# Kernel optimization log

Hardware: AMD Instinct MI355X
Metric: run time of the kernel (lower is better)

The kernel has to match this reference:

```python
import jax, jax.numpy as jnp
import numpy as np

NUM_HEADS = 16
HEAD_DIM = 64
D_MODEL = NUM_HEADS * HEAD_DIM
DFF = 4096
LN_EPS = 1e-3  # keras LayerNormalization default epsilon


def layer_norm(x, gamma, beta):
    mu = jnp.mean(x, axis=-1, keepdims=True)
    var = jnp.mean(jnp.square(x - mu), axis=-1, keepdims=True)
    return (x - mu) * jax.lax.rsqrt(var + LN_EPS) * gamma + beta


def setup_inputs() -> dict:
    key = jax.random.key(0)
    ks = jax.random.split(key, 8)
    N, T = 2, 2048
    s = 0.02
    return {
        "x": jax.random.normal(ks[0], (N, T, D_MODEL), dtype=jnp.float32),
        "mask": jnp.ones((N, T), dtype=jnp.float32),
        "w_qkv": jax.random.normal(ks[1], (D_MODEL, 3 * D_MODEL), dtype=jnp.float32) * s,
        "b_qkv": jnp.zeros((3 * D_MODEL,), dtype=jnp.float32),
        "w_ff": jax.random.normal(ks[2], (D_MODEL, DFF), dtype=jnp.float32) * s,
        "b_ff": jnp.zeros((DFF,), dtype=jnp.float32),
        "w_out": jax.random.normal(ks[3], (DFF, D_MODEL), dtype=jnp.float32) * s,
        "b_out": jnp.zeros((D_MODEL,), dtype=jnp.float32),
        "ln1_g": jnp.ones((D_MODEL,), dtype=jnp.float32),
        "ln1_b": jnp.zeros((D_MODEL,), dtype=jnp.float32),
        "ln2_g": jnp.ones((D_MODEL,), dtype=jnp.float32),
        "ln2_b": jnp.zeros((D_MODEL,), dtype=jnp.float32),
    }


def reference(x, mask, w_qkv, b_qkv, w_ff, b_ff, w_out, b_out, ln1_g, ln1_b, ln2_g, ln2_b):
    N, T, _ = x.shape
    H, D = NUM_HEADS, HEAD_DIM
    # --- MHA ---
    qkv = x @ w_qkv + b_qkv                     # [N, T, 3*H*D]
    qkv = qkv.reshape(N, T, H, D, 3)
    qkv = jnp.transpose(qkv, (4, 0, 2, 1, 3))   # [3, N, H, T, D]
    q, k, v = qkv[0], qkv[1], qkv[2]
    logits = jnp.einsum('nhqd,nhkd->nhqk', q, k) * (1.0 / (D ** 0.5))
    # NB: faithful to original: mask[:, None, :, None] masks the QUERY axis
    logits = logits + (1.0 - mask[:, None, :, None]) * -1e9
    attn = jax.nn.softmax(logits, axis=-1)
    ctx = jnp.einsum('nhqk,nhkd->nhqd', attn, v)  # [N, H, T, D]
    ctx = jnp.transpose(ctx, (0, 2, 1, 3)).reshape(N, T, H * D)
    # dropout_rc1: identity (training=False)
    h = layer_norm(x + ctx, ln1_g, ln1_b)
    # --- FFN ---
    ff = jax.nn.relu(h @ w_ff + b_ff)             # [N, T, DFF]
    out = layer_norm(h + ff @ w_out + b_out, ln2_g, ln2_b)
    return out
```

## Files before the change

### kernel.cpp

```cpp
#include <hip/hip_runtime.h>
#include <hip/hip_fp8.h>
#include <stdint.h>

#define DM    1024
#define DFFN  4096
#define NTOK  4096
#define TT    2048
#define NHEAD 16
#define HD    64
#define LN_EPS 1e-3f
#define QSCALE 0.18033688011112042f

typedef float  f32x4  __attribute__((ext_vector_type(4)));
typedef __bf16 bf16x8 __attribute__((ext_vector_type(8)));

using void_as1 = __attribute__((address_space(1))) void;
using void_as3 = __attribute__((address_space(3))) void;

__device__ __forceinline__ void g2l16(const void* g, void* l) {
    __builtin_amdgcn_global_load_lds((const void_as1*)g, (void_as3*)l, 16, 0, 0);
}

__device__ __forceinline__ unsigned short f2bf(float f) {
    unsigned u = __builtin_bit_cast(unsigned, f);
    u += 0x7FFFu + ((u >> 16) & 1u);
    return (unsigned short)(u >> 16);
}

__device__ __forceinline__ float fexp2(float x) {
#if __has_builtin(__builtin_amdgcn_exp2f)
    return __builtin_amdgcn_exp2f(x);
#else
    return exp2f(x);
#endif
}

template <bool HI>
__device__ __forceinline__ unsigned cvt2fp8(float a, float b, unsigned old) {
#if __has_builtin(__builtin_amdgcn_cvt_pk_fp8_f32)
    return (unsigned)__builtin_amdgcn_cvt_pk_fp8_f32(a, b, (int)old, HI);
#else
    __hip_fp8_e4m3 ta(a), tb(b);
    unsigned w = (unsigned)ta.__x | ((unsigned)tb.__x << 8);
    return HI ? ((old & 0x0000FFFFu) | (w << 16)) : ((old & 0xFFFF0000u) | w);
#endif
}

__device__ __forceinline__ unsigned char f2fp8(float f) {
    return (unsigned char)(cvt2fp8<false>(f, 0.f, 0u) & 0xffu);
}

__global__ __launch_bounds__(256) void cast_bf16_kernel(
    const float* __restrict__ in, unsigned short* __restrict__ out, int n4) {
    int i = blockIdx.x * 256 + threadIdx.x;
    if (i < n4) {
        float4 v = ((const float4*)in)[i];
        ushort4 o;
        o.x = f2bf(v.x); o.y = f2bf(v.y); o.z = f2bf(v.z); o.w = f2bf(v.w);
        ((ushort4*)out)[i] = o;
    }
}

__global__ __launch_bounds__(256) void transpose_cast_kernel(
    const float* __restrict__ w, unsigned short* __restrict__ wT, int K, int Nc) {
    __shared__ float tile[32][33];
    int tx = threadIdx.x & 31, ty = threadIdx.x >> 5;
    int n0 = blockIdx.x * 32, k0 = blockIdx.y * 32;
#pragma unroll
    for (int i = 0; i < 4; ++i)
        tile[ty + 8 * i][tx] = w[(size_t)(k0 + ty + 8 * i) * Nc + (n0 + tx)];
    __syncthreads();
#pragma unroll
    for (int i = 0; i < 4; ++i)
        wT[(size_t)(n0 + ty + 8 * i) * K + (k0 + tx)] = f2bf(tile[tx][ty + 8 * i]);
}

template <int EPI>
__global__ __launch_bounds__(256, 4) void gemm_bt_kernel(
    const unsigned short* __restrict__ A,
    const unsigned short* __restrict__ Bt,
    const float* __restrict__ bias,
    unsigned short* __restrict__ oq,
    unsigned short* __restrict__ ok,
    unsigned short* __restrict__ ov,
    float* __restrict__ of,
    int K, int Ksplit) {
    __shared__ unsigned short As[128 * 64];
    __shared__ unsigned short Bs[128 * 64];
    const int tid  = threadIdx.x;
    const int wave = tid >> 6, lane = tid & 63;
    const int quad = lane >> 4, l16 = lane & 15;
    const int sw = l16 & 7;
    const int wm = wave >> 1, wn = wave & 1;
    const int nBase = blockIdx.x * 128, mBase = blockIdx.y * 128;
    const int kb = blockIdx.z * Ksplit, ke = kb + Ksplit;

    f32x4 acc[4][4] = {};

    for (int k0 = kb; k0 < ke; k0 += 64) {
#pragma unroll
        for (int i = 0; i < 4; ++i) {
            const int chunk = i * 256 + tid;
            const int row = chunk >> 3, kc = chunk & 7;
            const int kl = kc ^ (row & 7);
            g2l16(A  + (size_t)(mBase + row) * K + (k0 + kl * 8),
                  (char*)As + (size_t)(i * 256 + wave * 64) * 16);
        }
#pragma unroll
        for (int i = 0; i < 4; ++i) {
            const int chunk = i * 256 + tid;
            const int row = chunk >> 3, kc = chunk & 7;
            const int kl = kc ^ (row & 7);
            g2l16(Bt + (size_t)(nBase + row) * K + (k0 + kl * 8),
                  (char*)Bs + (size_t)(i * 256 + wave * 64) * 16);
        }
        __syncthreads();
#pragma unroll
        for (int ks = 0; ks < 2; ++ks) {
            bf16x8 af[4], bfr[4];
#pragma unroll
            for (int i = 0; i < 4; ++i)
                af[i] = *(const bf16x8*)(const void*)(
                    As + (wm * 64 + i * 16 + l16) * 64 + (((ks * 4 + quad) ^ sw) << 3));
#pragma unroll
            for (int j = 0; j < 4; ++j)
                bfr[j] = *(const bf16x8*)(const void*)(
                    Bs + (wn * 64 + j * 16 + l16) * 64 + (((ks * 4 + quad) ^ sw) << 3));
#pragma unroll
            for (int i = 0; i < 4; ++i)
#pragma unroll
                for (int j = 0; j < 4; ++j)
                    acc[i][j] = __builtin_amdgcn_mfma_f32_16x16x32_bf16(af[i], bfr[j], acc[i][j], 0, 0, 0);
        }
        __syncthreads();
    }

    float* dst2 = (EPI == 2) ? (blockIdx.z ? (float*)ov : of) : nullptr;

#pragma unroll
    for (int i = 0; i < 4; ++i) {
        const int rbase = mBase + wm * 64 + i * 16 + quad * 4;
#pragma unroll
        for (int j = 0; j < 4; ++j) {
            const int col = nBase + wn * 64 + j * 16 + l16;
            const float bv = (EPI == 2) ? 0.0f : bias[col];
#pragma unroll
            for (int r = 0; r < 4; ++r) {
                const int row = rbase + r;
                const float v = acc[i][j][r] + bv;
                if (EPI == 0) {
                    const int h = col / 192;
                    const int rem = col - h * 192;
                    const int d = rem / 3;
                    const int s = rem - d * 3;
                    const int n = row >> 11, t = row & (TT - 1);
                    const int nh = n * NHEAD + h;
                    if (s == 0)
                        ((unsigned char*)oq)[((size_t)nh * TT + t) * HD + d] = f2fp8(v);
                    else if (s == 1)
                        ((unsigned char*)ok)[((size_t)nh * TT + t) * HD + d] = f2fp8(v);
                    else {
                        const int tl = t & 127;
                        const int tp = ((tl & 15) << 3) | (tl >> 4);
                        ((unsigned char*)ov)[((size_t)nh * HD + d) * TT + (t & ~127) + tp] = f2fp8(v);
                    }
                } else if (EPI == 1) {
                    oq[(size_t)row * DFFN + col] = f2bf(fmaxf(v, 0.0f));
                } else {
                    dst2[(size_t)row * DM + col] = v;
                }
            }
        }
    }
}

#define PST 136
__global__ __launch_bounds__(512, 4) void attn_kernel(
    const unsigned char* __restrict__ q,
    const unsigned char* __restrict__ k,
    const unsigned char* __restrict__ vt,
    float* __restrict__ ctx) {
    __shared__ __align__(16) unsigned char Ks[128 * 64];
    __shared__ __align__(16) unsigned char Vs[64 * 128];
    __shared__ __align__(16) unsigned char Plds[8][16 * PST];
    const int tid  = threadIdx.x;
    const int wave = tid >> 6, lane = tid & 63;
    const int quad = lane >> 4, l16 = lane & 15;
    const int nh = blockIdx.x & 31;
    const int qt = blockIdx.x >> 5;
    const unsigned char* qh = q  + (size_t)nh * TT * HD;
    const unsigned char* kh = k  + (size_t)nh * TT * HD;
    const unsigned char* vh = vt + (size_t)nh * HD * TT;

    const int qrow = qt * 128 + wave * 16;
    const long qa0 = *(const long*)(const void*)(qh + (size_t)(qrow + l16) * HD + quad * 8);
    const long qa1 = *(const long*)(const void*)(qh + (size_t)(qrow + l16) * HD + 32 + quad * 8);

    f32x4 o[4] = {};
    f32x4 rs = {};
    unsigned char* pw = &Plds[wave][0];
    const int sw2 = (l16 >> 1) & 3;

    for (int kt = 0; kt < TT; kt += 128) {
        {
            const int r = wave * 16 + (lane >> 2);
            const int lc = (lane & 3) ^ ((lane >> 3) & 3);
            g2l16(kh + (size_t)(kt + r) * HD + lc * 16, (char*)Ks + wave * 1024);
        }
        {
            const int d = wave * 8 + (lane >> 3);
            const int lc = (lane & 7) ^ (d & 7);
            g2l16(vh + (size_t)d * TT + kt + lc * 16, (char*)Vs + wave * 1024);
        }
        __syncthreads();

        f32x4 s[8];
#pragma unroll
        for (int c = 0; c < 8; ++c) {
            const int r = c * 16 + l16;
            const long kb0 = *(const long*)(const void*)(
                Ks + r * 64 + ((((quad >> 1) ^ sw2)) << 4) + ((quad & 1) << 3));
            const long kb1 = *(const long*)(const void*)(
                Ks + r * 64 + (((2 + (quad >> 1)) ^ sw2) << 4) + ((quad & 1) << 3));
            f32x4 z = {};
            z = __builtin_amdgcn_mfma_f32_16x16x32_fp8_fp8(qa0, kb0, z, 0, 0, 0);
            s[c] = __builtin_amdgcn_mfma_f32_16x16x32_fp8_fp8(qa1, kb1, z, 0, 0, 0);
        }
#pragma unroll
        for (int c = 0; c < 8; ++c)
#pragma unroll
            for (int r = 0; r < 4; ++r) {
                float p = fexp2(s[c][r] * QSCALE);
                s[c][r] = p;
                rs[r] += p;
            }
#pragma unroll
        for (int r = 0; r < 4; ++r) {
            const int row = quad * 4 + r;
            unsigned lo = cvt2fp8<false>(s[0][r], s[1][r], 0u);
            lo = cvt2fp8<true>(s[2][r], s[3][r], lo);
            unsigned hi = cvt2fp8<false>(s[4][r], s[5][r], 0u);
            hi = cvt2fp8<true>(s[6][r], s[7][r], hi);
            uint2 wv; wv.x = lo; wv.y = hi;
            *(uint2*)(void*)(pw + row * PST + l16 * 8) = wv;
        }
        asm volatile("s_waitcnt lgkmcnt(0)" ::: "memory");
#pragma unroll
        for (int kc = 0; kc < 4; ++kc) {
            const long pa = *(const long*)(const void*)(pw + l16 * PST + kc * 32 + quad * 8);
#pragma unroll
            for (int dc = 0; dc < 4; ++dc) {
                const int physc = (kc * 2 + (quad >> 1)) ^ (l16 & 7);
                const long vb = *(const long*)(const void*)(
                    Vs + (dc * 16 + l16) * 128 + physc * 16 + ((quad & 1) << 3));
                o[dc] = __builtin_amdgcn_mfma_f32_16x16x32_fp8_fp8(pa, vb, o[dc], 0, 0, 0);
            }
        }
        __syncthreads();
    }

    const int n = nh >> 4, h = nh & 15;
#pragma unroll
    for (int r = 0; r < 4; ++r) {
        float t = rs[r];
        t += __shfl_xor(t, 1, 64);
        t += __shfl_xor(t, 2, 64);
        t += __shfl_xor(t, 4, 64);
        t += __shfl_xor(t, 8, 64);
        const float inv = 1.0f / t;
        const int trow = qrow + quad * 4 + r;
        float* op = ctx + ((size_t)(n * TT + trow)) * DM + h * HD;
#pragma unroll
        for (int dc = 0; dc < 4; ++dc)
            op[dc * 16 + l16] = o[dc][r] * inv;
    }
}

__global__ __launch_bounds__(256) void add_ln_kernel(
    const float* __restrict__ a, const float* __restrict__ b,
    const float* __restrict__ c, const float* __restrict__ cbias,
    const float* __restrict__ gamma, const float* __restrict__ beta,
    float* __restrict__ outf, unsigned short* __restrict__ outb) {
    const int row = blockIdx.x;
    const int tid = threadIdx.x;
    const int lane = tid & 63, wave = tid >> 6;
    const float4 av = ((const float4*)(a + (size_t)row * DM))[tid];
    const float4 bv = ((const float4*)(b + (size_t)row * DM))[tid];
    float4 x;
    x.x = av.x + bv.x; x.y = av.y + bv.y; x.z = av.z + bv.z; x.w = av.w + bv.w;
    if (c) {
        const float4 cv = ((const float4*)(c + (size_t)row * DM))[tid];
        const float4 cb = ((const float4*)cbias)[tid];
        x.x += cv.x + cb.x; x.y += cv.y + cb.y; x.z += cv.z + cb.z; x.w += cv.w + cb.w;
    }
    float s = x.x + x.y + x.z + x.w;
    float q = x.x * x.x + x.y * x.y + x.z * x.z + x.w * x.w;
#pragma unroll
    for (int off = 1; off < 64; off <<= 1) {
        s += __shfl_xor(s, off, 64);
        q += __shfl_xor(q, off, 64);
    }
    __shared__ float sh[8];
    if (lane == 0) { sh[wave] = s; sh[4 + wave] = q; }
    __syncthreads();
    s = sh[0] + sh[1] + sh[2] + sh[3];
    q = sh[4] + sh[5] + sh[6] + sh[7];
    const float mu = s * (1.0f / DM);
    const float var = q * (1.0f / DM) - mu * mu;
    const float rstd = rsqrtf(var + LN_EPS);
    const float4 g4 = ((const float4*)gamma)[tid];
    const float4 b4 = ((const float4*)beta)[tid];
    float4 o;
    o.x = (x.x - mu) * rstd * g4.x + b4.x;
    o.y = (x.y - mu) * rstd * g4.y + b4.y;
    o.z = (x.z - mu) * rstd * g4.z + b4.z;
    o.w = (x.w - mu) * rstd * g4.w + b4.w;
    ((float4*)(outf + (size_t)row * DM))[tid] = o;
    if (outb) {
        ushort4 ob;
        ob.x = f2bf(o.x); ob.y = f2bf(o.y); ob.z = f2bf(o.z); ob.w = f2bf(o.w);
        ((ushort4*)(outb + (size_t)row * DM))[tid] = ob;
    }
}

extern "C" void kernel_launch(void* const* d_in, const int* in_sizes, int n_in,
                              void* d_out, int out_size, void* d_ws, size_t ws_size,
                              hipStream_t stream) {
    const float* x     = (const float*)d_in[0];
    const float* w_qkv = (const float*)d_in[2];
    const float* b_qkv = (const float*)d_in[3];
    const float* w_ff  = (const float*)d_in[4];
    const float* b_ff  = (const float*)d_in[5];
    const float* w_out = (const float*)d_in[6];
    const float* b_out = (const float*)d_in[7];
    const float* ln1_g = (const float*)d_in[8];
    const float* ln1_b = (const float*)d_in[9];
    const float* ln2_g = (const float*)d_in[10];
    const float* ln2_b = (const float*)d_in[11];

    char* ws = (char*)d_ws;
    unsigned short* xb    = (unsigned short*)(ws);
    unsigned short* wqkvT = (unsigned short*)(ws + 8388608);
    unsigned short* wffT  = (unsigned short*)(ws + 14680064);
    unsigned short* woutT = (unsigned short*)(ws + 23068672);
    unsigned char*  qb    = (unsigned char*)(ws + 31457280);
    unsigned char*  kb    = (unsigned char*)(ws + 39845888);
    unsigned char*  vtb   = (unsigned char*)(ws + 48234496);
    float*          ctx   = (float*)(ws + 56623104);
    float*          hbuf  = (float*)(ws + 73400320);
    unsigned short* hb    = (unsigned short*)(ws + 90177536);
    unsigned short* ffb   = (unsigned short*)(ws + 98566144);
    float*          tmp   = (float*)(ws + 132120576);

    cast_bf16_kernel<<<(NTOK * DM / 4 + 255) / 256, 256, 0, stream>>>(x, xb, NTOK * DM / 4);
    transpose_cast_kernel<<<dim3(3072 / 32, DM / 32), 256, 0, stream>>>(w_qkv, wqkvT, DM, 3072);
    transpose_cast_kernel<<<dim3(DFFN / 32, DM / 32), 256, 0, stream>>>(w_ff, wffT, DM, DFFN);
    transpose_cast_kernel<<<dim3(DM / 32, DFFN / 32), 256, 0, stream>>>(w_out, woutT, DFFN, DM);

    gemm_bt_kernel<0><<<dim3(3072 / 128, NTOK / 128), 256, 0, stream>>>(
        xb, wqkvT, b_qkv, (unsigned short*)qb, (unsigned short*)kb,
        (unsigned short*)vtb, nullptr, DM, DM);

    attn_kernel<<<512, 512, 0, stream>>>(qb, kb, vtb, ctx);

    add_ln_kernel<<<NTOK, 256, 0, stream>>>(x, ctx, nullptr, nullptr,
                                            ln1_g, ln1_b, hbuf, hb);

    gemm_bt_kernel<1><<<dim3(DFFN / 128, NTOK / 128), 256, 0, stream>>>(
        hb, wffT, b_ff, ffb, nullptr, nullptr, nullptr, DM, DM);

    gemm_bt_kernel<2><<<dim3(DM / 128, NTOK / 128, 2), 256, 0, stream>>>(
        ffb, woutT, nullptr, nullptr, nullptr, (unsigned short*)ctx, tmp, DFFN, DFFN / 2);

    add_ln_kernel<<<NTOK, 256, 0, stream>>>(hbuf, tmp, ctx, b_out,
                                            ln2_g, ln2_b, (float*)d_out, nullptr);
}
```

Before: 328.4 us.

## Run QKV projection in FP8 and give each attention wave 32 query rows

The QKV projection now runs as a dedicated FP8 GEMM. Its input is cast to FP8, and the weights are pre-permuted so each output column maps directly to q/k/v, head and dim, which makes the scatter epilogue cheaper. The attention kernel now uses 256 threads per block, and each wave processes two 16-row query sub-tiles against the shared K/V tiles. This doubles K/V reuse per LDS load, and the P buffer uses a swizzled layout instead of padding. The risks are lower QKV accuracy from FP8 inputs and weights, and higher register pressure in attention.

```diff
diff --git a/kernel.cpp b/kernel.cpp
--- a/kernel.cpp
+++ b/kernel.cpp
@@ -13,6 +13,7 @@
 
 typedef float  f32x4  __attribute__((ext_vector_type(4)));
 typedef __bf16 bf16x8 __attribute__((ext_vector_type(8)));
+typedef long   lx2    __attribute__((ext_vector_type(2)));
 
 using void_as1 = __attribute__((address_space(1))) void;
 using void_as3 = __attribute__((address_space(3))) void;
@@ -50,14 +51,14 @@
     return (unsigned char)(cvt2fp8<false>(f, 0.f, 0u) & 0xffu);
 }
 
-__global__ __launch_bounds__(256) void cast_bf16_kernel(
-    const float* __restrict__ in, unsigned short* __restrict__ out, int n4) {
+__global__ __launch_bounds__(256) void cast_fp8_kernel(
+    const float* __restrict__ in, unsigned char* __restrict__ out, int n4) {
     int i = blockIdx.x * 256 + threadIdx.x;
     if (i < n4) {
         float4 v = ((const float4*)in)[i];
-        ushort4 o;
-        o.x = f2bf(v.x); o.y = f2bf(v.y); o.z = f2bf(v.z); o.w = f2bf(v.w);
-        ((ushort4*)out)[i] = o;
+        unsigned p = cvt2fp8<false>(v.x, v.y, 0u);
+        p = cvt2fp8<true>(v.z, v.w, p);
+        ((unsigned*)out)[i] = p;
     }
 }
 
@@ -75,15 +76,120 @@
         wT[(size_t)(n0 + ty + 8 * i) * K + (k0 + tx)] = f2bf(tile[tx][ty + 8 * i]);
 }
 
+__global__ __launch_bounds__(256) void transpose_qkv_fp8_kernel(
+    const float* __restrict__ w, unsigned char* __restrict__ wT) {
+    __shared__ float tile[32][33];
+    int tx = threadIdx.x & 31, ty = threadIdx.x >> 5;
+    int c0 = blockIdx.x * 32, k0 = blockIdx.y * 32;
+#pragma unroll
+    for (int i = 0; i < 4; ++i)
+        tile[ty + 8 * i][tx] = w[(size_t)(k0 + ty + 8 * i) * 3072 + (c0 + tx)];
+    __syncthreads();
+#pragma unroll
+    for (int i = 0; i < 4; ++i) {
+        const int col = c0 + ty + 8 * i;
+        const int h = col / 192;
+        const int rem = col - h * 192;
+        const int d = rem / 3;
+        const int s = rem - d * 3;
+        const int colp = s * 1024 + h * 64 + d;
+        wT[(size_t)colp * 1024 + (k0 + tx)] = f2fp8(tile[tx][ty + 8 * i]);
+    }
+}
+
+__global__ __launch_bounds__(256, 4) void gemm_qkv_fp8_kernel(
+    const unsigned char* __restrict__ A,
+    const unsigned char* __restrict__ Bt,
+    const float* __restrict__ bias,
+    unsigned char* __restrict__ oq,
+    unsigned char* __restrict__ ok,
+    unsigned char* __restrict__ ov) {
+    __shared__ __align__(16) unsigned char As[128 * 64];
+    __shared__ __align__(16) unsigned char Bs[128 * 64];
+    const int tid  = threadIdx.x;
+    const int wave = tid >> 6, lane = tid & 63;
+    const int quad = lane >> 4, l16 = lane & 15;
+    const int sw2 = (l16 >> 1) & 3;
+    const int wm = wave >> 1, wn = wave & 1;
+    const int nBase = blockIdx.x * 128, mBase = blockIdx.y * 128;
+
+    f32x4 acc[4][4] = {};
+
+    for (int k0 = 0; k0 < 1024; k0 += 64) {
+#pragma unroll
+        for (int i = 0; i < 2; ++i) {
+            const int chunk = i * 256 + tid;
+            const int row = chunk >> 2, p = chunk & 3;
+            const int l = p ^ ((row >> 1) & 3);
+            g2l16(A + (size_t)(mBase + row) * 1024 + (k0 + l * 16),
+                  (char*)As + (size_t)(i * 256 + wave * 64) * 16);
+        }
+#pragma unroll
+        for (int i = 0; i < 2; ++i) {
+            const int chunk = i * 256 + tid;
+            const int row = chunk >> 2, p = chunk & 3;
+            const int l = p ^ ((row >> 1) & 3);
+            g2l16(Bt + (size_t)(nBase + row) * 1024 + (k0 + l * 16),
+                  (char*)Bs + (size_t)(i * 256 + wave * 64) * 16);
+        }
+        __syncthreads();
+        lx2 af[4], bf[4];
+#pragma unroll
+        for (int i = 0; i < 4; ++i)
+            af[i] = *(const lx2*)(const void*)(
+                As + (wm * 64 + i * 16 + l16) * 64 + ((quad ^ sw2) << 4));
+#pragma unroll
+        for (int j = 0; j < 4; ++j)
+            bf[j] = *(const lx2*)(const void*)(
+                Bs + (wn * 64 + j * 16 + l16) * 64 + ((quad ^ sw2) << 4));
+#pragma unroll
+        for (int i = 0; i < 4; ++i)
+#pragma unroll
+            for (int j = 0; j < 4; ++j) {
+                acc[i][j] = __builtin_amdgcn_mfma_f32_16x16x32_fp8_fp8(af[i].x, bf[j].x, acc[i][j], 0, 0, 0);
+                acc[i][j] = __builtin_amdgcn_mfma_f32_16x16x32_fp8_fp8(af[i].y, bf[j].y, acc[i][j], 0, 0, 0);
+            }
+        __syncthreads();
+    }
+
+#pragma unroll
+    for (int i = 0; i < 4; ++i) {
+        const int rbase = mBase + wm * 64 + i * 16 + quad * 4;
+#pragma unroll
+        for (int j = 0; j < 4; ++j) {
+            const int colp = nBase + wn * 64 + j * 16 + l16;
+            const int s = colp >> 10;
+            const int h = (colp >> 6) & 15;
+            const int d = colp & 63;
+            const float bv = bias[h * 192 + d * 3 + s];
+#pragma unroll
+            for (int r = 0; r < 4; ++r) {
+                const int row = rbase + r;
+                const float v = acc[i][j][r] + bv;
+                const int n = row >> 11, t = row & (TT - 1);
+                const int nh = n * NHEAD + h;
+                if (s == 0)
+                    oq[((size_t)nh * TT + t) * HD + d] = f2fp8(v);
+                else if (s == 1)
+                    ok[((size_t)nh * TT + t) * HD + d] = f2fp8(v);
+                else {
+                    const int tl = t & 127;
+                    const int tp = ((tl & 15) << 3) | (tl >> 4);
+                    ov[((size_t)nh * HD + d) * TT + (t & ~127) + tp] = f2fp8(v);
+                }
+            }
+        }
+    }
+}
+
 template <int EPI>
 __global__ __launch_bounds__(256, 4) void gemm_bt_kernel(
     const unsigned short* __restrict__ A,
     const unsigned short* __restrict__ Bt,
     const float* __restrict__ bias,
-    unsigned short* __restrict__ oq,
-    unsigned short* __restrict__ ok,
-    unsigned short* __restrict__ ov,
+    unsigned short* __restrict__ ob,
     float* __restrict__ of,
+    float* __restrict__ of2,
     int K, int Ksplit) {
     __shared__ unsigned short As[128 * 64];
     __shared__ unsigned short Bs[128 * 64];
@@ -135,7 +241,7 @@
         __syncthreads();
     }
 
-    float* dst2 = (EPI == 2) ? (blockIdx.z ? (float*)ov : of) : nullptr;
+    float* dst2 = (EPI == 2) ? (blockIdx.z ? of2 : of) : nullptr;
 
 #pragma unroll
     for (int i = 0; i < 4; ++i) {
@@ -148,132 +254,133 @@
             for (int r = 0; r < 4; ++r) {
                 const int row = rbase + r;
                 const float v = acc[i][j][r] + bv;
-                if (EPI == 0) {
-                    const int h = col / 192;
-                    const int rem = col - h * 192;
-                    const int d = rem / 3;
-                    const int s = rem - d * 3;
-                    const int n = row >> 11, t = row & (TT - 1);
-                    const int nh = n * NHEAD + h;
-                    if (s == 0)
-                        ((unsigned char*)oq)[((size_t)nh * TT + t) * HD + d] = f2fp8(v);
-                    else if (s == 1)
-                        ((unsigned char*)ok)[((size_t)nh * TT + t) * HD + d] = f2fp8(v);
-                    else {
-                        const int tl = t & 127;
-                        const int tp = ((tl & 15) << 3) | (tl >> 4);
-                        ((unsigned char*)ov)[((size_t)nh * HD + d) * TT + (t & ~127) + tp] = f2fp8(v);
-                    }
-                } else if (EPI == 1) {
-                    oq[(size_t)row * DFFN + col] = f2bf(fmaxf(v, 0.0f));
-                } else {
+                if (EPI == 1)
+                    ob[(size_t)row * DFFN + col] = f2bf(fmaxf(v, 0.0f));
+                else
                     dst2[(size_t)row * DM + col] = v;
-                }
-            }
-        }
-    }
-}
-
-#define PST 136
-__global__ __launch_bounds__(512, 4) void attn_kernel(
+            }
+        }
+    }
+}
+
+__global__ __launch_bounds__(256, 4) void attn_kernel(
     const unsigned char* __restrict__ q,
     const unsigned char* __restrict__ k,
     const unsigned char* __restrict__ vt,
     float* __restrict__ ctx) {
     __shared__ __align__(16) unsigned char Ks[128 * 64];
     __shared__ __align__(16) unsigned char Vs[64 * 128];
-    __shared__ __align__(16) unsigned char Plds[8][16 * PST];
+    __shared__ __align__(16) unsigned char Plds[4][32 * 128];
     const int tid  = threadIdx.x;
     const int wave = tid >> 6, lane = tid & 63;
     const int quad = lane >> 4, l16 = lane & 15;
+    const int sw2 = (l16 >> 1) & 3;
+    const int sw3 = l16 & 7;
     const int nh = blockIdx.x & 31;
     const int qt = blockIdx.x >> 5;
     const unsigned char* qh = q  + (size_t)nh * TT * HD;
     const unsigned char* kh = k  + (size_t)nh * TT * HD;
     const unsigned char* vh = vt + (size_t)nh * HD * TT;
 
-    const int qrow = qt * 128 + wave * 16;
-    const long qa0 = *(const long*)(const void*)(qh + (size_t)(qrow + l16) * HD + quad * 8);
-    const long qa1 = *(const long*)(const void*)(qh + (size_t)(qrow + l16) * HD + 32 + quad * 8);
-
-    f32x4 o[4] = {};
-    f32x4 rs = {};
+    const int qrow = qt * 128 + wave * 32;
+    lx2 qa[2];
+#pragma unroll
+    for (int sub = 0; sub < 2; ++sub)
+        qa[sub] = *(const lx2*)(const void*)(
+            qh + (size_t)(qrow + sub * 16 + l16) * HD + quad * 16);
+
+    f32x4 o[2][4] = {};
+    f32x4 rs[2] = {};
     unsigned char* pw = &Plds[wave][0];
-    const int sw2 = (l16 >> 1) & 3;
 
     for (int kt = 0; kt < TT; kt += 128) {
-        {
-            const int r = wave * 16 + (lane >> 2);
+#pragma unroll
+        for (int i = 0; i < 2; ++i) {
+            const int widx = i * 4 + wave;
+            const int r = widx * 16 + (lane >> 2);
             const int lc = (lane & 3) ^ ((lane >> 3) & 3);
-            g2l16(kh + (size_t)(kt + r) * HD + lc * 16, (char*)Ks + wave * 1024);
-        }
-        {
-            const int d = wave * 8 + (lane >> 3);
-            const int lc = (lane & 7) ^ (d & 7);
-            g2l16(vh + (size_t)d * TT + kt + lc * 16, (char*)Vs + wave * 1024);
-        }
-        __syncthreads();
-
-        f32x4 s[8];
-#pragma unroll
-        for (int c = 0; c < 8; ++c) {
-            const int r = c * 16 + l16;
-            const long kb0 = *(const long*)(const void*)(
-                Ks + r * 64 + ((((quad >> 1) ^ sw2)) << 4) + ((quad & 1) << 3));
-            const long kb1 = *(const long*)(const void*)(
-                Ks + r * 64 + (((2 + (quad >> 1)) ^ sw2) << 4) + ((quad & 1) << 3));
-            f32x4 z = {};
-            z = __builtin_amdgcn_mfma_f32_16x16x32_fp8_fp8(qa0, kb0, z, 0, 0, 0);
-            s[c] = __builtin_amdgcn_mfma_f32_16x16x32_fp8_fp8(qa1, kb1, z, 0, 0, 0);
-        }
-#pragma unroll
-        for (int c = 0; c < 8; ++c)
+            g2l16(kh + (size_t)(kt + r) * HD + lc * 16, (char*)Ks + widx * 1024);
+        }
+#pragma unroll
+        for (int i = 0; i < 2; ++i) {
+            const int widx = i * 4 + wave;
+            const int d = widx * 8 + (lane >> 3);
+            const int lc = (lane & 7) ^ ((lane >> 3) & 7);
+            g2l16(vh + (size_t)d * TT + kt + lc * 16, (char*)Vs + widx * 1024);
+        }
+        __syncthreads();
+
+#pragma unroll
+        for (int sub = 0; sub < 2; ++sub) {
+            f32x4 s[8];
+#pragma unroll
+            for (int c = 0; c < 8; ++c) {
+                const int r = c * 16 + l16;
+                const lx2 kb = *(const lx2*)(const void*)(
+                    Ks + r * 64 + ((quad ^ sw2) << 4));
+                f32x4 z = {};
+                z = __builtin_amdgcn_mfma_f32_16x16x32_fp8_fp8(qa[sub].x, kb.x, z, 0, 0, 0);
+                s[c] = __builtin_amdgcn_mfma_f32_16x16x32_fp8_fp8(qa[sub].y, kb.y, s[c] = z, 0, 0, 0);
+            }
+#pragma unroll
+            for (int c = 0; c < 8; ++c)
+#pragma unroll
+                for (int r = 0; r < 4; ++r) {
+                    float p = fexp2(s[c][r] * QSCALE);
+                    s[c][r] = p;
+                    rs[sub][r] += p;
+                }
 #pragma unroll
             for (int r = 0; r < 4; ++r) {
-                float p = fexp2(s[c][r] * QSCALE);
-                s[c][r] = p;
-                rs[r] += p;
-            }
+                const int row = sub * 16 + quad * 4 + r;
+                const int physc = (l16 >> 1) ^ (row & 7);
+                unsigned lo = cvt2fp8<false>(s[0][r], s[1][r], 0u);
+                lo = cvt2fp8<true>(s[2][r], s[3][r], lo);
+                unsigned hi = cvt2fp8<false>(s[4][r], s[5][r], 0u);
+                hi = cvt2fp8<true>(s[6][r], s[7][r], hi);
+                uint2 wv; wv.x = lo; wv.y = hi;
+                *(uint2*)(void*)(pw + row * 128 + physc * 16 + ((l16 & 1) << 3)) = wv;
+            }
+        }
+        asm volatile("s_waitcnt lgkmcnt(0)" ::: "memory");
+#pragma unroll
+        for (int m = 0; m < 2; ++m) {
+            lx2 pa[2];
+#pragma unroll
+            for (int sub = 0; sub < 2; ++sub)
+                pa[sub] = *(const lx2*)(const void*)(
+                    pw + (sub * 16 + l16) * 128 + (((m * 4 + quad) ^ sw3) << 4));
+#pragma unroll
+            for (int dc = 0; dc < 4; ++dc) {
+                const lx2 vb = *(const lx2*)(const void*)(
+                    Vs + (dc * 16 + l16) * 128 + (((m * 4 + quad) ^ sw3) << 4));
+#pragma unroll
+                for (int sub = 0; sub < 2; ++sub) {
+                    o[sub][dc] = __builtin_amdgcn_mfma_f32_16x16x32_fp8_fp8(pa[sub].x, vb.x, o[sub][dc], 0, 0, 0);
+                    o[sub][dc] = __builtin_amdgcn_mfma_f32_16x16x32_fp8_fp8(pa[sub].y, vb.y, o[sub][dc], 0, 0, 0);
+                }
+            }
+        }
+        __syncthreads();
+    }
+
+    const int n = nh >> 4, h = nh & 15;
+#pragma unroll
+    for (int sub = 0; sub < 2; ++sub)
 #pragma unroll
         for (int r = 0; r < 4; ++r) {
-            const int row = quad * 4 + r;
-            unsigned lo = cvt2fp8<false>(s[0][r], s[1][r], 0u);
-            lo = cvt2fp8<true>(s[2][r], s[3][r], lo);
-            unsigned hi = cvt2fp8<false>(s[4][r], s[5][r], 0u);
-            hi = cvt2fp8<true>(s[6][r], s[7][r], hi);
-            uint2 wv; wv.x = lo; wv.y = hi;
-            *(uint2*)(void*)(pw + row * PST + l16 * 8) = wv;
-        }
-        asm volatile("s_waitcnt lgkmcnt(0)" ::: "memory");
-#pragma unroll
-        for (int kc = 0; kc < 4; ++kc) {
-            const long pa = *(const long*)(const void*)(pw + l16 * PST + kc * 32 + quad * 8);
-#pragma unroll
-            for (int dc = 0; dc < 4; ++dc) {
-                const int physc = (kc * 2 + (quad >> 1)) ^ (l16 & 7);
-                const long vb = *(const long*)(const void*)(
-                    Vs + (dc * 16 + l16) * 128 + physc * 16 + ((quad & 1) << 3));
-                o[dc] = __builtin_amdgcn_mfma_f32_16x16x32_fp8_fp8(pa, vb, o[dc], 0, 0, 0);
-            }
-        }
-        __syncthreads();
-    }
-
-    const int n = nh >> 4, h = nh & 15;
-#pragma unroll
-    for (int r = 0; r < 4; ++r) {
-        float t = rs[r];
-        t += __shfl_xor(t, 1, 64);
-        t += __shfl_xor(t, 2, 64);
-        t += __shfl_xor(t, 4, 64);
-        t += __shfl_xor(t, 8, 64);
-        const float inv = 1.0f / t;
-        const int trow = qrow + quad * 4 + r;
-        float* op = ctx + ((size_t)(n * TT + trow)) * DM + h * HD;
-#pragma unroll
-        for (int dc = 0; dc < 4; ++dc)
-            op[dc * 16 + l16] = o[dc][r] * inv;
-    }
+            float t = rs[sub][r];
+            t += __shfl_xor(t, 1, 64);
+            t += __shfl_xor(t, 2, 64);
+            t += __shfl_xor(t, 4, 64);
+            t += __shfl_xor(t, 8, 64);
+            const float inv = 1.0f / t;
+            const int trow = qrow + sub * 16 + quad * 4 + r;
+            float* op = ctx + ((size_t)(n * TT + trow)) * DM + h * HD;
+#pragma unroll
+            for (int dc = 0; dc < 4; ++dc)
+                op[dc * 16 + l16] = o[sub][dc][r] * inv;
+        }
 }
 
 __global__ __launch_bounds__(256) void add_ln_kernel(
@@ -339,8 +446,8 @@
     const float* ln2_b = (const float*)d_in[11];
 
     char* ws = (char*)d_ws;
-    unsigned short* xb    = (unsigned short*)(ws);
-    unsigned short* wqkvT = (unsigned short*)(ws + 8388608);
+    unsigned char*  x8    = (unsigned char*)(ws);
+    unsigned char*  wq8   = (unsigned char*)(ws + 8388608);
     unsigned short* wffT  = (unsigned short*)(ws + 14680064);
     unsigned short* woutT = (unsigned short*)(ws + 23068672);
     unsigned char*  qb    = (unsigned char*)(ws + 31457280);
@@ -352,25 +459,24 @@
     unsigned short* ffb   = (unsigned short*)(ws + 98566144);
     float*          tmp   = (float*)(ws + 132120576);
 
-    cast_bf16_kernel<<<(NTOK * DM / 4 + 255) / 256, 256, 0, stream>>>(x, xb, NTOK * DM / 4);
-    transpose_cast_kernel<<<dim3(3072 / 32, DM / 32), 256, 0, stream>>>(w_qkv, wqkvT, DM, 3072);
+    cast_fp8_kernel<<<(NTOK * DM / 4 + 255) / 256, 256, 0, stream>>>(x, x8, NTOK * DM / 4);
+    transpose_qkv_fp8_kernel<<<dim3(3072 / 32, DM / 32), 256, 0, stream>>>(w_qkv, wq8);
     transpose_cast_kernel<<<dim3(DFFN / 32, DM / 32), 256, 0, stream>>>(w_ff, wffT, DM, DFFN);
     transpose_cast_kernel<<<dim3(DM / 32, DFFN / 32), 256, 0, stream>>>(w_out, woutT, DFFN, DM);
 
-    gemm_bt_kernel<0><<<dim3(3072 / 128, NTOK / 128), 256, 0, stream>>>(
-        xb, wqkvT, b_qkv, (unsigned short*)qb, (unsigned short*)kb,
-        (unsigned short*)vtb, nullptr, DM, DM);
-
-    attn_kernel<<<512, 512, 0, stream>>>(qb, kb, vtb, ctx);
+    gemm_qkv_fp8_kernel<<<dim3(3072 / 128, NTOK / 128), 256, 0, stream>>>(
+        x8, wq8, b_qkv, qb, kb, vtb);
+
+    attn_kernel<<<512, 256, 0, stream>>>(qb, kb, vtb, ctx);
 
     add_ln_kernel<<<NTOK, 256, 0, stream>>>(x, ctx, nullptr, nullptr,
                                             ln1_g, ln1_b, hbuf, hb);
 
     gemm_bt_kernel<1><<<dim3(DFFN / 128, NTOK / 128), 256, 0, stream>>>(
-        hb, wffT, b_ff, ffb, nullptr, nullptr, nullptr, DM, DM);
+        hb, wffT, b_ff, ffb, nullptr, nullptr, DM, DM);
 
     gemm_bt_kernel<2><<<dim3(DM / 128, NTOK / 128, 2), 256, 0, stream>>>(
-        ffb, woutT, nullptr, nullptr, nullptr, (unsigned short*)ctx, tmp, DFFN, DFFN / 2);
+        ffb, woutT, nullptr, nullptr, tmp, ctx, DFFN, DFFN / 2);
 
     add_ln_kernel<<<NTOK, 256, 0, stream>>>(hbuf, tmp, ctx, b_out,
                                             ln2_g, ln2_b, (float*)d_out, nullptr);
```

Result: faster. 306.3 us (-6.7%).
